# Kernel tuning notes

Measured on AMD Instinct MI355X. Metric: run time of the kernel, lower is better.

## Reference

```python
import jax, jax.numpy as jnp
import numpy as np

B, P, D = 16, 512, 1024   # batch, num wordpieces, bert_dim (roberta-large)
W, T, E = 400, 32, 64     # num words, num triggers (spans), num entities (spans)
H = 600                   # hidden_num of role_idn_ffn


def _make_idxs(rng, b, m, n, max_len):
    # [start, end) intervals with 0 <= start < end <= n, sorted starts per row
    starts = np.sort(rng.integers(0, n - 1, size=(b, m)), axis=1)
    ends = np.minimum(starts + rng.integers(1, max_len + 1, size=(b, m)), n)
    ends = np.maximum(ends, starts + 1)
    return np.stack([starts, ends], axis=-1).astype(np.int32)


def setup_inputs() -> dict:
    key = jax.random.key(0)
    k1, k2, k3 = jax.random.split(key, 3)
    rng = np.random.default_rng(0)
    return {
        "piece_reprs": jax.random.normal(k1, (B, P, D), dtype=jnp.float32),
        "word_idxs": jnp.asarray(_make_idxs(rng, B, W, P, 4)),
        "trigger_idxs": jnp.asarray(_make_idxs(rng, B, T, W, 8)),
        "entity_idxs": jnp.asarray(_make_idxs(rng, B, E, W, 12)),
        "W0": jax.random.normal(k2, (4 * D, H), dtype=jnp.float32) * 0.02,
        "b0": jnp.zeros((H,), dtype=jnp.float32),
        "W1": jax.random.normal(k3, (H, 2), dtype=jnp.float32) * 0.02,
        "b1": jnp.zeros((2,), dtype=jnp.float32),
    }


def _segment_mean(x, idxs):
    """Mean of x[b, start:end] per interval. x: [B,N,Dm], idxs: [B,M,2] -> [B,M,Dm].
    Vectorized replacement of the nested-loop slice+mean via inclusive prefix sums."""
    cs = jnp.concatenate([jnp.zeros_like(x[:, :1]), jnp.cumsum(x, axis=1)], axis=1)  # [B,N+1,Dm]
    s = jnp.take_along_axis(cs, idxs[:, :, 0:1], axis=1)  # [B,M,Dm]
    e = jnp.take_along_axis(cs, idxs[:, :, 1:2], axis=1)  # [B,M,Dm]
    lens = (idxs[:, :, 1] - idxs[:, :, 0]).astype(x.dtype)[:, :, None]
    return (e - s) / lens


def reference(piece_reprs, word_idxs, trigger_idxs, entity_idxs, W0, b0, W1, b1):
    # encode(): wordpiece -> word averaging (compute_word_reps_avg)
    word_reprs = _segment_mean(piece_reprs, word_idxs)          # [B, W, D]
    # scores(): span mean pooling (compute_span_reprs)
    trig = _segment_mean(word_reprs, trigger_idxs)              # [B, T, D]
    ent = _segment_mean(word_reprs, entity_idxs)                # [B, E, D]
    b, t, d = trig.shape
    e = ent.shape[1]
    # compute_binary_reprs: all (trigger, entity) pairs, trigger index varies slowly
    t_rep = jnp.broadcast_to(trig[:, :, None, :], (b, t, e, d)).reshape(b, t * e, d)
    e_rep = jnp.broadcast_to(ent[:, None, :, :], (b, t, e, d)).reshape(b, t * e, d)
    role = jnp.concatenate([t_rep, e_rep, t_rep * e_rep, jnp.abs(t_rep - e_rep)], axis=-1)  # [B,T*E,4D]
    # role_idn_ffn: Linears([4D, H, 2]) with relu between layers (dropout=0 at eval)
    h = jax.nn.relu(role @ W0 + b0)
    return h @ W1 + b1                                          # [B, T*E, 2]
```

## Files before the change

kernel.cpp:

```cpp
#include <hip/hip_runtime.h>
#include <cstddef>
#include <cstdint>

typedef float f32x4 __attribute__((ext_vector_type(4)));
typedef __bf16 bf16x8 __attribute__((ext_vector_type(8)));

constexpr int NB = 16;
constexpr int NP = 512;
constexpr int ND = 1024;
constexpr int NW = 400;
constexpr int NT = 32;
constexpr int NE = 64;
constexpr int NH = 600;
constexpr int IMGP = 128 * 64;
constexpr int IMGQ = 160 * 32;

__device__ inline bf16x8 pack8(float a0, float a1, float a2, float a3,
                               float a4, float a5, float a6, float a7) {
    bf16x8 v;
    v[0] = (__bf16)a0; v[1] = (__bf16)a1; v[2] = (__bf16)a2; v[3] = (__bf16)a3;
    v[4] = (__bf16)a4; v[5] = (__bf16)a5; v[6] = (__bf16)a6; v[7] = (__bf16)a7;
    return v;
}

__device__ inline void dma16(const void* g, void* l) {
    __builtin_amdgcn_global_load_lds(
        (const __attribute__((address_space(1))) uint32_t*)g,
        (__attribute__((address_space(3))) uint32_t*)l, 16, 0, 0);
}

__global__ __launch_bounds__(256) void word_mean_kernel(
    const float* __restrict__ piece, const int* __restrict__ widx,
    float* __restrict__ word) {
    int bw = blockIdx.x;
    int b = bw / NW;
    int s = widx[bw * 2], e = widx[bw * 2 + 1];
    int col = threadIdx.x * 4;
    const float* base = piece + (size_t)b * NP * ND + col;
    float4 acc = make_float4(0.f, 0.f, 0.f, 0.f);
    for (int r = s; r < e; ++r) {
        float4 v = *(const float4*)(base + (size_t)r * ND);
        acc.x += v.x; acc.y += v.y; acc.z += v.z; acc.w += v.w;
    }
    float inv = 1.0f / (float)(e - s);
    acc.x *= inv; acc.y *= inv; acc.z *= inv; acc.w *= inv;
    *(float4*)(word + (size_t)bw * ND + col) = acc;
}

__global__ __launch_bounds__(256) void span_mean_kernel(
    const float* __restrict__ word, const int* __restrict__ tidx,
    const int* __restrict__ eidx, float* __restrict__ trig,
    float* __restrict__ ent) {
    int id = blockIdx.x;
    const int* idx;
    float* out;
    int b;
    if (id < NB * NT) {
        b = id / NT; idx = tidx + id * 2; out = trig + (size_t)id * ND;
    } else {
        int id2 = id - NB * NT;
        b = id2 / NE; idx = eidx + id2 * 2; out = ent + (size_t)id2 * ND;
    }
    int s = idx[0], e = idx[1];
    int col = threadIdx.x * 4;
    const float* base = word + (size_t)b * NW * ND + col;
    float4 acc = make_float4(0.f, 0.f, 0.f, 0.f);
    for (int r = s; r < e; ++r) {
        float4 v = *(const float4*)(base + (size_t)r * ND);
        acc.x += v.x; acc.y += v.y; acc.z += v.z; acc.w += v.w;
    }
    float inv = 1.0f / (float)(e - s);
    acc.x *= inv; acc.y *= inv; acc.z *= inv; acc.w *= inv;
    *(float4*)(out + col) = acc;
}

__global__ __launch_bounds__(256) void w0_build_kernel(
    const float* __restrict__ W0, __bf16* __restrict__ W0pre,
    __bf16* __restrict__ W0pair) {
    __shared__ float T[64][132];
    int id = blockIdx.x;
    int t = threadIdx.x;
    if (id < 160) {
        int kb = id & 31, nc = id >> 5;
        {
            int kl = t >> 2;
            int n0 = (t & 3) * 32;
            int kg = kb * 64 + kl;
            const float* src = W0 + (size_t)kg * NH + nc * 128 + n0;
#pragma unroll
            for (int g = 0; g < 8; ++g) {
                int n = nc * 128 + n0 + g * 4;
                float4 v = (n < NH) ? *(const float4*)(src + g * 4)
                                    : make_float4(0.f, 0.f, 0.f, 0.f);
                *(float4*)&T[kl][n0 + g * 4] = v;
            }
        }
        __syncthreads();
#pragma unroll
        for (int s = 0; s < 4; ++s) {
            int idx = t * 4 + s;
            int row = idx >> 3, c = idx & 7;
            bf16x8 v = pack8(T[c * 8 + 0][row], T[c * 8 + 1][row],
                             T[c * 8 + 2][row], T[c * 8 + 3][row],
                             T[c * 8 + 4][row], T[c * 8 + 5][row],
                             T[c * 8 + 6][row], T[c * 8 + 7][row]);
            __bf16* img = W0pre + ((size_t)nc * 32 + kb) * IMGP;
            *(bf16x8*)&img[row * 64 + ((c ^ (row & 7)) << 3)] = v;
        }
    } else {
        int e = id - 160;
        int it = e & 63, z = e >> 6;
        float (*Tp)[164] = reinterpret_cast<float(*)[164]>(&T[0][0]);
        {
            int k = t >> 3, seg = t & 7;
            int korig = (k < 16) ? (2048 + it * 16 + k)
                                 : (3072 + it * 16 + (k - 16));
            const float* src = W0 + (size_t)korig * NH;
#pragma unroll
            for (int g = 0; g < 5; ++g) {
                int n = z * 160 + seg * 20 + g * 4;
                float4 v = (n < NH) ? *(const float4*)(src + n)
                                    : make_float4(0.f, 0.f, 0.f, 0.f);
                *(float4*)&Tp[k][seg * 20 + g * 4] = v;
            }
        }
        __syncthreads();
        __bf16* img = W0pair + ((size_t)z * 64 + it) * IMGQ;
#pragma unroll
        for (int s = 0; s < 3; ++s) {
            int idx = s * 256 + t;
            if (idx < 640) {
                int r = idx >> 2, c = idx & 3;
                bf16x8 v = pack8(Tp[c * 8 + 0][r], Tp[c * 8 + 1][r],
                                 Tp[c * 8 + 2][r], Tp[c * 8 + 3][r],
                                 Tp[c * 8 + 4][r], Tp[c * 8 + 5][r],
                                 Tp[c * 8 + 6][r], Tp[c * 8 + 7][r]);
                int slot = ((r >> 1) + c) & 3;
                *(bf16x8*)&img[r * 32 + slot * 8] = v;
            }
        }
    }
}

__global__ __launch_bounds__(256) void pre_mfma_kernel(
    const float* __restrict__ trig, const float* __restrict__ ent,
    const __bf16* __restrict__ W0pre, float* __restrict__ pre_t,
    float* __restrict__ pre_e) {
    __shared__ __bf16 As[64 * 64];
    __shared__ __bf16 Bs[64 * 64];
    int mt8 = blockIdx.x, ntile = blockIdx.y;
    const float* A;
    float* C;
    int kbofs, mbase;
    if (mt8 < 8) { A = trig; C = pre_t; kbofs = 0;  mbase = mt8 * 64; }
    else         { A = ent;  C = pre_e; kbofs = 16; mbase = (mt8 - 8) * 64; }
    int tid = threadIdx.x;
    int lane = tid & 63, w = tid >> 6, rw = w & 1, cw = w >> 1;
    int q = lane >> 4, l15 = lane & 15, sa = l15 & 7;
    int nc = ntile >> 1, half = ntile & 1;
    const __bf16* imgbase =
        W0pre + ((size_t)nc * 32 + kbofs) * IMGP + half * 4096;
    int ar = tid >> 2, seg = tid & 3;
    f32x4 acc[2][2] = {};

    for (int it = 0; it < 16; ++it) {
        __syncthreads();
        const __bf16* img = imgbase + (size_t)it * IMGP;
#pragma unroll
        for (int i = 0; i < 2; ++i) {
            int idx = i * 4 + w;
            dma16(img + idx * 512 + lane * 8, (__bf16*)Bs + idx * 512);
        }
        {
            const float* src = A + (size_t)(mbase + ar) * ND + it * 64;
#pragma unroll
            for (int i = 0; i < 2; ++i) {
                int c = seg * 2 + i;
                float4 a0 = *(const float4*)(src + c * 8);
                float4 a1 = *(const float4*)(src + c * 8 + 4);
                *(bf16x8*)&As[ar * 64 + ((c ^ (ar & 7)) << 3)] =
                    pack8(a0.x, a0.y, a0.z, a0.w, a1.x, a1.y, a1.z, a1.w);
            }
        }
        __syncthreads();
#pragma unroll
        for (int ks = 0; ks < 2; ++ks) {
            int coff = ((q ^ sa) ^ (ks << 2)) << 3;
            bf16x8 af[2];
#pragma unroll
            for (int mt = 0; mt < 2; ++mt)
                af[mt] = *(const bf16x8*)&As[(32 * rw + 16 * mt + l15) * 64 + coff];
#pragma unroll
            for (int nt = 0; nt < 2; ++nt) {
                bf16x8 bf = *(const bf16x8*)&Bs[(32 * cw + 16 * nt + l15) * 64 + coff];
#pragma unroll
                for (int mt = 0; mt < 2; ++mt)
                    acc[mt][nt] = __builtin_amdgcn_mfma_f32_16x16x32_bf16(
                        af[mt], bf, acc[mt][nt], 0, 0, 0);
            }
        }
    }
#pragma unroll
    for (int mt = 0; mt < 2; ++mt)
#pragma unroll
        for (int r = 0; r < 4; ++r) {
            float* crow =
                C + (size_t)(mbase + 32 * rw + 16 * mt + 4 * q + r) * NH;
#pragma unroll
            for (int nt = 0; nt < 2; ++nt) {
                int n = ntile * 64 + 32 * cw + 16 * nt + l15;
                if (n < NH) crow[n] = acc[mt][nt][r];
            }
        }
}

__global__ __launch_bounds__(256, 4) void pair_mfma_kernel(
    const float* __restrict__ trig, const float* __restrict__ ent,
    const __bf16* __restrict__ W0pair, const float* __restrict__ b0,
    const float* __restrict__ pre_t, const float* __restrict__ pre_e,
    const float* __restrict__ W1, const float* __restrict__ b1,
    float* __restrict__ out) {
    __shared__ __bf16 Xs[2][128 * 32];
    __shared__ __bf16 Bs[2][160 * 32];
    __shared__ __bf16 Ts[2048];
    int b = blockIdx.x, tp = blockIdx.y, z = blockIdx.z;
    int tid = threadIdx.x;
    int lane = tid & 63, w = tid >> 6, rw = w & 1, cw = w >> 1;
    int q = lane >> 4, l15 = lane & 15;
    int xr = tid >> 1, xh = tid & 1;
    const float* t0row = trig + (size_t)(b * NT + tp * 2) * ND;
    const float* erow = ent + (size_t)(b * NE + (xr & 63)) * ND;
    const __bf16* imgbase = W0pair + (size_t)z * 64 * IMGQ;
    f32x4 acc[4][5] = {};
    float4 ef4[2];

    auto dma_b = [&](int it, int buf) {
        const __bf16* img = imgbase + (size_t)it * IMGQ;
        __bf16* lds = Bs[buf];
#pragma unroll
        for (int i = 0; i < 3; ++i) {
            int idx = i * 4 + w;
            if (idx < 10)
                dma16(img + idx * 512 + lane * 8, lds + idx * 512);
        }
    };
    auto load_e = [&](int it) {
        const float* er = erow + it * 16 + xh * 8;
        ef4[0] = *(const float4*)er;
        ef4[1] = *(const float4*)(er + 4);
    };
    auto write_x = [&](int it, int buf) {
        bf16x8 tv = *(const bf16x8*)&Ts[(xr >> 6) * 1024 + it * 16 + xh * 8];
        float tf[8], ef[8];
#pragma unroll
        for (int j = 0; j < 8; ++j) tf[j] = (float)tv[j];
        ef[0] = ef4[0].x; ef[1] = ef4[0].y; ef[2] = ef4[0].z; ef[3] = ef4[0].w;
        ef[4] = ef4[1].x; ef[5] = ef4[1].y; ef[6] = ef4[1].z; ef[7] = ef4[1].w;
        int sp = (((xr >> 1) + xh) & 3) * 8;
        int sd = (((xr >> 1) + 2 + xh) & 3) * 8;
        __bf16* xb = &Xs[buf][xr * 32];
        *(bf16x8*)(xb + sp) = pack8(
            tf[0] * ef[0], tf[1] * ef[1], tf[2] * ef[2], tf[3] * ef[3],
            tf[4] * ef[4], tf[5] * ef[5], tf[6] * ef[6], tf[7] * ef[7]);
        *(bf16x8*)(xb + sd) = pack8(
            fabsf(tf[0] - ef[0]), fabsf(tf[1] - ef[1]),
            fabsf(tf[2] - ef[2]), fabsf(tf[3] - ef[3]),
            fabsf(tf[4] - ef[4]), fabsf(tf[5] - ef[5]),
            fabsf(tf[6] - ef[6]), fabsf(tf[7] - ef[7]));
    };
    auto mfma_tile = [&](int buf) {
        const __bf16* X = Xs[buf];
        const __bf16* Bb = Bs[buf];
        bf16x8 af[4];
#pragma unroll
        for (int mt = 0; mt < 4; ++mt) {
            int r = 64 * rw + 16 * mt + l15;
            af[mt] = *(const bf16x8*)&X[r * 32 + (((r >> 1) + q) & 3) * 8];
        }
#pragma unroll
        for (int nt = 0; nt < 5; ++nt) {
            int r = 80 * cw + 16 * nt + l15;
            bf16x8 bv = *(const bf16x8*)&Bb[r * 32 + (((r >> 1) + q) & 3) * 8];
#pragma unroll
            for (int mt = 0; mt < 4; ++mt)
                acc[mt][nt] = __builtin_amdgcn_mfma_f32_16x16x32_bf16(
                    af[mt], bv, acc[mt][nt], 0, 0, 0);
        }
    };

    {
        int k0 = (tid & 127) * 8;
        const float* src = t0row + (tid >> 7) * ND + k0;
        float4 va = *(const float4*)src;
        float4 vb = *(const float4*)(src + 4);
        *(bf16x8*)&Ts[tid * 8] =
            pack8(va.x, va.y, va.z, va.w, vb.x, vb.y, vb.z, vb.w);
    }
    dma_b(0, 0);
    load_e(0);
    __syncthreads();
    write_x(0, 0);
    __syncthreads();

    for (int it = 0; it < 64; ++it) {
        int cur = it & 1, nxt = cur ^ 1;
        if (it < 63) {
            load_e(it + 1);
            dma_b(it + 1, nxt);
        }
        mfma_tile(cur);
        if (it < 63) write_x(it + 1, nxt);
        __syncthreads();
    }

    int tglob = b * NT + tp * 2 + rw;
    const float* preT = pre_t + (size_t)tglob * NH;
    float w10[5], w11[5], b0v[5], ptv[5];
    int nbase = z * 160 + 80 * cw + l15;
#pragma unroll
    for (int nt = 0; nt < 5; ++nt) {
        int n = nbase + 16 * nt;
        bool v = n < NH;
        w10[nt] = v ? W1[2 * n] : 0.f;
        w11[nt] = v ? W1[2 * n + 1] : 0.f;
        b0v[nt] = v ? b0[n] : 0.f;
        ptv[nt] = v ? preT[n] : 0.f;
    }
    float b10 = b1[0], b11 = b1[1];
    bool lead = (l15 == 0);
    bool addb = (z == 0) && (cw == 0);
#pragma unroll
    for (int mt = 0; mt < 4; ++mt) {
#pragma unroll
        for (int r = 0; r < 4; ++r) {
            int e = 16 * mt + 4 * q + r;
            const float* preE = pre_e + (size_t)(b * NE + e) * NH;
            float s0 = 0.f, s1 = 0.f;
#pragma unroll
            for (int nt = 0; nt < 5; ++nt) {
                int n = nbase + 16 * nt;
                float pe = (n < NH) ? preE[n] : 0.f;
                float h = acc[mt][nt][r] + ptv[nt] + pe + b0v[nt];
                h = fmaxf(h, 0.f);
                s0 += h * w10[nt];
                s1 += h * w11[nt];
            }
#pragma unroll
            for (int m = 8; m >= 1; m >>= 1) {
                s0 += __shfl_xor(s0, m);
                s1 += __shfl_xor(s1, m);
            }
            if (lead) {
                if (addb) { s0 += b10; s1 += b11; }
                float* o = out + ((size_t)(tglob * NE + e)) * 2;
                atomicAdd(o, s0);
                atomicAdd(o + 1, s1);
            }
        }
    }
}

extern "C" void kernel_launch(void* const* d_in, const int* in_sizes, int n_in,
                              void* d_out, int out_size, void* d_ws,
                              size_t ws_size, hipStream_t stream) {
    const float* piece = (const float*)d_in[0];
    const int* widx = (const int*)d_in[1];
    const int* tidx = (const int*)d_in[2];
    const int* eidx = (const int*)d_in[3];
    const float* W0 = (const float*)d_in[4];
    const float* b0 = (const float*)d_in[5];
    const float* W1 = (const float*)d_in[6];
    const float* b1 = (const float*)d_in[7];
    float* out = (float*)d_out;

    float* ws = (float*)d_ws;
    float* word = ws;
    float* trig = word + (size_t)NB * NW * ND;
    float* ent = trig + (size_t)NB * NT * ND;
    float* pre_t = ent + (size_t)NB * NE * ND;
    float* pre_e = pre_t + (size_t)NB * NT * NH;
    __bf16* W0pre = (__bf16*)word;
    __bf16* W0pair = W0pre + (size_t)5 * 32 * IMGP;

    hipMemsetAsync(d_out, 0, (size_t)out_size * sizeof(float), stream);

    word_mean_kernel<<<NB * NW, 256, 0, stream>>>(piece, widx, word);
    span_mean_kernel<<<NB * (NT + NE), 256, 0, stream>>>(word, tidx, eidx, trig, ent);
    w0_build_kernel<<<416, 256, 0, stream>>>(W0, W0pre, W0pair);
    pre_mfma_kernel<<<dim3(24, 10), 256, 0, stream>>>(trig, ent, W0pre, pre_t, pre_e);
    pair_mfma_kernel<<<dim3(16, 16, 4), 256, 0, stream>>>(
        trig, ent, W0pair, b0, pre_t, pre_e, W1, b1, out);
}
```

Before: 233.8 us.

## Fuse word and span means, merge output zeroing, widen pair tile N

```diff
diff --git a/kernel.cpp b/kernel.cpp
--- a/kernel.cpp
+++ b/kernel.cpp
@@ -13,7 +13,7 @@
 constexpr int NE = 64;
 constexpr int NH = 600;
 constexpr int IMGP = 128 * 64;
-constexpr int IMGQ = 160 * 32;
+constexpr int IMGQ = 320 * 32;
 
 __device__ inline bf16x8 pack8(float a0, float a1, float a2, float a3,
                                float a4, float a5, float a6, float a7) {
@@ -29,54 +29,44 @@
         (__attribute__((address_space(3))) uint32_t*)l, 16, 0, 0);
 }
 
-__global__ __launch_bounds__(256) void word_mean_kernel(
+__global__ __launch_bounds__(256) void span_mean_kernel(
     const float* __restrict__ piece, const int* __restrict__ widx,
-    float* __restrict__ word) {
-    int bw = blockIdx.x;
-    int b = bw / NW;
-    int s = widx[bw * 2], e = widx[bw * 2 + 1];
+    const int* __restrict__ tidx, const int* __restrict__ eidx,
+    float* __restrict__ trig, float* __restrict__ ent) {
+    int id = blockIdx.x;
+    const int* idx;
+    float* outp;
+    int b;
+    if (id < NB * NT) {
+        b = id / NT; idx = tidx + id * 2; outp = trig + (size_t)id * ND;
+    } else {
+        int id2 = id - NB * NT;
+        b = id2 / NE; idx = eidx + id2 * 2; outp = ent + (size_t)id2 * ND;
+    }
+    int s = idx[0], e = idx[1];
     int col = threadIdx.x * 4;
-    const float* base = piece + (size_t)b * NP * ND + col;
+    const int* wrow = widx + b * NW * 2;
+    const float* pbase = piece + (size_t)b * NP * ND + col;
     float4 acc = make_float4(0.f, 0.f, 0.f, 0.f);
-    for (int r = s; r < e; ++r) {
-        float4 v = *(const float4*)(base + (size_t)r * ND);
-        acc.x += v.x; acc.y += v.y; acc.z += v.z; acc.w += v.w;
+    for (int w = s; w < e; ++w) {
+        int ps = wrow[2 * w], pe = wrow[2 * w + 1];
+        float4 wa = make_float4(0.f, 0.f, 0.f, 0.f);
+        for (int p = ps; p < pe; ++p) {
+            float4 v = *(const float4*)(pbase + (size_t)p * ND);
+            wa.x += v.x; wa.y += v.y; wa.z += v.z; wa.w += v.w;
+        }
+        float wi = 1.0f / (float)(pe - ps);
+        acc.x += wa.x * wi; acc.y += wa.y * wi;
+        acc.z += wa.z * wi; acc.w += wa.w * wi;
     }
     float inv = 1.0f / (float)(e - s);
     acc.x *= inv; acc.y *= inv; acc.z *= inv; acc.w *= inv;
-    *(float4*)(word + (size_t)bw * ND + col) = acc;
-}
-
-__global__ __launch_bounds__(256) void span_mean_kernel(
-    const float* __restrict__ word, const int* __restrict__ tidx,
-    const int* __restrict__ eidx, float* __restrict__ trig,
-    float* __restrict__ ent) {
-    int id = blockIdx.x;
-    const int* idx;
-    float* out;
-    int b;
-    if (id < NB * NT) {
-        b = id / NT; idx = tidx + id * 2; out = trig + (size_t)id * ND;
-    } else {
-        int id2 = id - NB * NT;
-        b = id2 / NE; idx = eidx + id2 * 2; out = ent + (size_t)id2 * ND;
-    }
-    int s = idx[0], e = idx[1];
-    int col = threadIdx.x * 4;
-    const float* base = word + (size_t)b * NW * ND + col;
-    float4 acc = make_float4(0.f, 0.f, 0.f, 0.f);
-    for (int r = s; r < e; ++r) {
-        float4 v = *(const float4*)(base + (size_t)r * ND);
-        acc.x += v.x; acc.y += v.y; acc.z += v.z; acc.w += v.w;
-    }
-    float inv = 1.0f / (float)(e - s);
-    acc.x *= inv; acc.y *= inv; acc.z *= inv; acc.w *= inv;
-    *(float4*)(out + col) = acc;
-}
-
-__global__ __launch_bounds__(256) void w0_build_kernel(
+    *(float4*)(outp + col) = acc;
+}
+
+__global__ __launch_bounds__(256) void build_kernel(
     const float* __restrict__ W0, __bf16* __restrict__ W0pre,
-    __bf16* __restrict__ W0pair) {
+    __bf16* __restrict__ W0pair, float* __restrict__ out, int out_size) {
     __shared__ float T[64][132];
     int id = blockIdx.x;
     int t = threadIdx.x;
@@ -107,37 +97,43 @@
             __bf16* img = W0pre + ((size_t)nc * 32 + kb) * IMGP;
             *(bf16x8*)&img[row * 64 + ((c ^ (row & 7)) << 3)] = v;
         }
+    } else if (id < 672) {
+        int e = id - 160;
+        int it = e & 63, nc = (e >> 6) & 1, zz = e >> 7;
+        float (*Tp)[84] = reinterpret_cast<float(*)[84]>(&T[0][0]);
+        {
+            int kidx = t >> 3, part = t & 7;
+            int korig = (kidx < 16) ? (2048 + it * 16 + kidx)
+                                    : (3072 + it * 16 + (kidx - 16));
+            const float* src = W0 + (size_t)korig * NH;
+#pragma unroll
+            for (int g = 0; g < 10; ++g) {
+                int n = nc * 320 + zz * 80 + part * 10 + g;
+                Tp[kidx][part * 10 + g] = (n < NH) ? src[n] : 0.0f;
+            }
+        }
+        __syncthreads();
+        __bf16* img = W0pair + ((size_t)nc * 64 + it) * IMGQ;
+#pragma unroll
+        for (int s = 0; s < 2; ++s) {
+            int idx = s * 256 + t;
+            if (idx < 320) {
+                int rloc = idx >> 2, c = idx & 3;
+                bf16x8 v = pack8(Tp[c * 8 + 0][rloc], Tp[c * 8 + 1][rloc],
+                                 Tp[c * 8 + 2][rloc], Tp[c * 8 + 3][rloc],
+                                 Tp[c * 8 + 4][rloc], Tp[c * 8 + 5][rloc],
+                                 Tp[c * 8 + 6][rloc], Tp[c * 8 + 7][rloc]);
+                int rg = zz * 80 + rloc;
+                int slot = ((rg >> 1) + c) & 3;
+                *(bf16x8*)&img[rg * 32 + slot * 8] = v;
+            }
+        }
     } else {
-        int e = id - 160;
-        int it = e & 63, z = e >> 6;
-        float (*Tp)[164] = reinterpret_cast<float(*)[164]>(&T[0][0]);
-        {
-            int k = t >> 3, seg = t & 7;
-            int korig = (k < 16) ? (2048 + it * 16 + k)
-                                 : (3072 + it * 16 + (k - 16));
-            const float* src = W0 + (size_t)korig * NH;
-#pragma unroll
-            for (int g = 0; g < 5; ++g) {
-                int n = z * 160 + seg * 20 + g * 4;
-                float4 v = (n < NH) ? *(const float4*)(src + n)
-                                    : make_float4(0.f, 0.f, 0.f, 0.f);
-                *(float4*)&Tp[k][seg * 20 + g * 4] = v;
-            }
-        }
-        __syncthreads();
-        __bf16* img = W0pair + ((size_t)z * 64 + it) * IMGQ;
-#pragma unroll
-        for (int s = 0; s < 3; ++s) {
-            int idx = s * 256 + t;
-            if (idx < 640) {
-                int r = idx >> 2, c = idx & 3;
-                bf16x8 v = pack8(Tp[c * 8 + 0][r], Tp[c * 8 + 1][r],
-                                 Tp[c * 8 + 2][r], Tp[c * 8 + 3][r],
-                                 Tp[c * 8 + 4][r], Tp[c * 8 + 5][r],
-                                 Tp[c * 8 + 6][r], Tp[c * 8 + 7][r]);
-                int slot = ((r >> 1) + c) & 3;
-                *(bf16x8*)&img[r * 32 + slot * 8] = v;
-            }
+        int j = ((id - 672) * 256 + t) * 8;
+        float4 z = make_float4(0.f, 0.f, 0.f, 0.f);
+        if (j + 8 <= out_size) {
+            *(float4*)(out + j) = z;
+            *(float4*)(out + j + 4) = z;
         }
     }
 }
@@ -214,35 +210,32 @@
         }
 }
 
-__global__ __launch_bounds__(256, 4) void pair_mfma_kernel(
+__global__ __launch_bounds__(256, 2) void pair_mfma_kernel(
     const float* __restrict__ trig, const float* __restrict__ ent,
     const __bf16* __restrict__ W0pair, const float* __restrict__ b0,
     const float* __restrict__ pre_t, const float* __restrict__ pre_e,
     const float* __restrict__ W1, const float* __restrict__ b1,
     float* __restrict__ out) {
     __shared__ __bf16 Xs[2][128 * 32];
-    __shared__ __bf16 Bs[2][160 * 32];
+    __shared__ __bf16 Bs[2][320 * 32];
     __shared__ __bf16 Ts[2048];
-    int b = blockIdx.x, tp = blockIdx.y, z = blockIdx.z;
+    int b = blockIdx.x, tp = blockIdx.y, nc = blockIdx.z;
     int tid = threadIdx.x;
     int lane = tid & 63, w = tid >> 6, rw = w & 1, cw = w >> 1;
     int q = lane >> 4, l15 = lane & 15;
     int xr = tid >> 1, xh = tid & 1;
     const float* t0row = trig + (size_t)(b * NT + tp * 2) * ND;
     const float* erow = ent + (size_t)(b * NE + (xr & 63)) * ND;
-    const __bf16* imgbase = W0pair + (size_t)z * 64 * IMGQ;
-    f32x4 acc[4][5] = {};
+    const __bf16* imgbase = W0pair + (size_t)nc * 64 * IMGQ;
+    f32x4 acc[4][10] = {};
     float4 ef4[2];
 
     auto dma_b = [&](int it, int buf) {
-        const __bf16* img = imgbase + (size_t)it * IMGQ;
-        __bf16* lds = Bs[buf];
-#pragma unroll
-        for (int i = 0; i < 3; ++i) {
-            int idx = i * 4 + w;
-            if (idx < 10)
-                dma16(img + idx * 512 + lane * 8, lds + idx * 512);
-        }
+        const __bf16* img = imgbase + (size_t)it * IMGQ + w * 2560;
+        __bf16* lds = &Bs[buf][w * 2560];
+#pragma unroll
+        for (int i = 0; i < 5; ++i)
+            dma16(img + i * 512 + lane * 8, lds + i * 512);
     };
     auto load_e = [&](int it) {
         const float* er = erow + it * 16 + xh * 8;
@@ -278,8 +271,8 @@
             af[mt] = *(const bf16x8*)&X[r * 32 + (((r >> 1) + q) & 3) * 8];
         }
 #pragma unroll
-        for (int nt = 0; nt < 5; ++nt) {
-            int r = 80 * cw + 16 * nt + l15;
+        for (int nt = 0; nt < 10; ++nt) {
+            int r = 160 * cw + 16 * nt + l15;
             bf16x8 bv = *(const bf16x8*)&Bb[r * 32 + (((r >> 1) + q) & 3) * 8];
 #pragma unroll
             for (int mt = 0; mt < 4; ++mt)
@@ -315,10 +308,10 @@
 
     int tglob = b * NT + tp * 2 + rw;
     const float* preT = pre_t + (size_t)tglob * NH;
-    float w10[5], w11[5], b0v[5], ptv[5];
-    int nbase = z * 160 + 80 * cw + l15;
-#pragma unroll
-    for (int nt = 0; nt < 5; ++nt) {
+    float w10[10], w11[10], b0v[10], ptv[10];
+    int nbase = nc * 320 + 160 * cw + l15;
+#pragma unroll
+    for (int nt = 0; nt < 10; ++nt) {
         int n = nbase + 16 * nt;
         bool v = n < NH;
         w10[nt] = v ? W1[2 * n] : 0.f;
@@ -328,7 +321,7 @@
     }
     float b10 = b1[0], b11 = b1[1];
     bool lead = (l15 == 0);
-    bool addb = (z == 0) && (cw == 0);
+    bool addb = (nc == 0) && (cw == 0);
 #pragma unroll
     for (int mt = 0; mt < 4; ++mt) {
 #pragma unroll
@@ -337,7 +330,7 @@
             const float* preE = pre_e + (size_t)(b * NE + e) * NH;
             float s0 = 0.f, s1 = 0.f;
 #pragma unroll
-            for (int nt = 0; nt < 5; ++nt) {
+            for (int nt = 0; nt < 10; ++nt) {
                 int n = nbase + 16 * nt;
                 float pe = (n < NH) ? preE[n] : 0.f;
                 float h = acc[mt][nt][r] + ptv[nt] + pe + b0v[nt];
@@ -374,20 +367,18 @@
     float* out = (float*)d_out;
 
     float* ws = (float*)d_ws;
-    float* word = ws;
-    float* trig = word + (size_t)NB * NW * ND;
+    float* trig = ws;
     float* ent = trig + (size_t)NB * NT * ND;
     float* pre_t = ent + (size_t)NB * NE * ND;
     float* pre_e = pre_t + (size_t)NB * NT * NH;
-    __bf16* W0pre = (__bf16*)word;
+    __bf16* W0pre = (__bf16*)(pre_e + (size_t)NB * NE * NH);
     __bf16* W0pair = W0pre + (size_t)5 * 32 * IMGP;
 
-    hipMemsetAsync(d_out, 0, (size_t)out_size * sizeof(float), stream);
-
-    word_mean_kernel<<<NB * NW, 256, 0, stream>>>(piece, widx, word);
-    span_mean_kernel<<<NB * (NT + NE), 256, 0, stream>>>(word, tidx, eidx, trig, ent);
-    w0_build_kernel<<<416, 256, 0, stream>>>(W0, W0pre, W0pair);
-    pre_mfma_kernel<<<dim3(24, 10), 256, 0, stream>>>(trig, ent, W0pre, pre_t, pre_e);
-    pair_mfma_kernel<<<dim3(16, 16, 4), 256, 0, stream>>>(
+    build_kernel<<<704, 256, 0, stream>>>(W0, W0pre, W0pair, out, out_size);
+    span_mean_kernel<<<NB * (NT + NE), 256, 0, stream>>>(
+        piece, widx, tidx, eidx, trig, ent);
+    pre_mfma_kernel<<<dim3(24, 10), 256, 0, stream>>>(trig, ent, W0pre,
+                                                      pre_t, pre_e);
+    pair_mfma_kernel<<<dim3(16, 16, 2), 256, 0, stream>>>(
         trig, ent, W0pair, b0, pre_t, pre_e, W1, b1, out);
 }
```

New measurement: 222.0 us. 5.0% less time.
